# Kernel optimization log

Measured on AMD Instinct MI355X. Metric: run time of the kernel, lower is better.

Reference implementation:

```python
import jax, jax.numpy as jnp
import numpy as np

H = 1024          # hidden size
NH = 16           # num heads
HD = H // NH      # head dim = 64
I = 4096          # intermediate size
EPS = 1e-5


def _layer_norm(x, g, b):
    m = jnp.mean(x, axis=-1, keepdims=True)
    v = jnp.mean(jnp.square(x - m), axis=-1, keepdims=True)
    return (x - m) * jax.lax.rsqrt(v + EPS) * g + b


def setup_inputs() -> dict:
    key = jax.random.key(0)
    ks = jax.random.split(key, 8)
    B, S = 16, 1025
    s = 0.02
    return {
        "hidden_states": jax.random.normal(ks[0], (B, S, H), dtype=jnp.float32),
        "norm1_g": jnp.ones((H,), jnp.float32),
        "norm1_b": jnp.zeros((H,), jnp.float32),
        "qkv_w": jax.random.normal(ks[1], (3 * H, H), jnp.float32) * s,
        "qkv_b": jnp.zeros((3 * H,), jnp.float32),
        "proj_w": jax.random.normal(ks[2], (H, H), jnp.float32) * s,
        "proj_b": jnp.zeros((H,), jnp.float32),
        "ls1": jnp.full((H,), 0.1, jnp.float32),
        "norm2_g": jnp.ones((H,), jnp.float32),
        "norm2_b": jnp.zeros((H,), jnp.float32),
        "fc1_w": jax.random.normal(ks[3], (I, H), jnp.float32) * s,
        "fc1_b": jnp.zeros((I,), jnp.float32),
        "fc2_w": jax.random.normal(ks[4], (H, I), jnp.float32) * s,
        "fc2_b": jnp.zeros((H,), jnp.float32),
        "ls2": jnp.full((H,), 0.1, jnp.float32),
    }


def reference(hidden_states, norm1_g, norm1_b, qkv_w, qkv_b, proj_w, proj_b,
              ls1, norm2_g, norm2_b, fc1_w, fc1_b, fc2_w, fc2_b, ls2):
    B, S, _ = hidden_states.shape
    scale = HD ** -0.5

    # ---- attention branch ----
    x = _layer_norm(hidden_states, norm1_g, norm1_b)
    qkv = x @ qkv_w.T + qkv_b                      # [B,S,3H]
    qkv = qkv.reshape(B, S, 3, NH, HD).transpose(2, 0, 3, 1, 4)  # [3,B,NH,S,HD]
    q, k, v = qkv[0], qkv[1], qkv[2]
    attn = jnp.einsum('bhqd,bhkd->bhqk', q, k) * scale
    attn = jax.nn.softmax(attn, axis=-1)
    out = jnp.einsum('bhqk,bhkd->bhqd', attn, v)   # [B,NH,S,HD]
    out = out.transpose(0, 2, 1, 3).reshape(B, S, H)
    out = out @ proj_w.T + proj_b
    hidden_states = hidden_states + ls1 * out

    # ---- MLP branch ----
    y = _layer_norm(hidden_states, norm2_g, norm2_b)
    y = jax.nn.gelu(y @ fc1_w.T + fc1_b, approximate=False)
    y = y @ fc2_w.T + fc2_b
    return hidden_states + ls2 * y
```

## Files before the change

### kernel.cpp

```cpp
#include <hip/hip_runtime.h>

typedef __bf16 bf16_t;
typedef bf16_t bf16x8 __attribute__((ext_vector_type(8)));
typedef bf16_t bf16x4 __attribute__((ext_vector_type(4)));
typedef float f32x4 __attribute__((ext_vector_type(4)));

#define S_LEN 1025
#define B_ROWS 1032
#define M_P 16512
#define SP 1152

__global__ __launch_bounds__(256) void cvt_kernel(const float* __restrict__ qkv_w,
                                                  const float* __restrict__ proj_w,
                                                  const float* __restrict__ fc1_w,
                                                  const float* __restrict__ fc2_w,
                                                  bf16_t* __restrict__ out) {
  const int i = blockIdx.x * 256 + threadIdx.x;
  const float* src;
  int j = i;
  if (j < 786432) src = qkv_w;
  else if ((j -= 786432) < 262144) src = proj_w;
  else if ((j -= 262144) < 1048576) src = fc1_w;
  else { j -= 1048576; src = fc2_w; }
  const float4 v = ((const float4*)src)[j];
  bf16x4 o;
  o[0] = (bf16_t)v.x; o[1] = (bf16_t)v.y; o[2] = (bf16_t)v.z; o[3] = (bf16_t)v.w;
  ((bf16x4*)out)[i] = o;
}

__global__ __launch_bounds__(256) void ln_kernel(const float* __restrict__ x,
                                                 const float* __restrict__ g,
                                                 const float* __restrict__ bta,
                                                 bf16_t* __restrict__ o) {
  const int s = blockIdx.x, bb = blockIdx.y;
  const int t = threadIdx.x;
  const float4 v = ((const float4*)(x + ((long)bb * S_LEN + s) * 1024))[t];
  float sm = v.x + v.y + v.z + v.w;
  float sq = v.x * v.x + v.y * v.y + v.z * v.z + v.w * v.w;
#pragma unroll
  for (int off = 32; off > 0; off >>= 1) {
    sm += __shfl_down(sm, off);
    sq += __shfl_down(sq, off);
  }
  __shared__ float red[16];
  const int w = t >> 6, lane = t & 63;
  if (lane == 0) { red[w] = sm; red[8 + w] = sq; }
  __syncthreads();
  if (t == 0) {
    const float ts = red[0] + red[1] + red[2] + red[3];
    const float tq = red[8] + red[9] + red[10] + red[11];
    const float mean = ts * (1.0f / 1024.0f);
    const float var = tq * (1.0f / 1024.0f) - mean * mean;
    red[0] = mean;
    red[1] = rsqrtf(var + 1e-5f);
  }
  __syncthreads();
  const float mean = red[0], rstd = red[1];
  const float4 gg = ((const float4*)g)[t];
  const float4 bb2 = ((const float4*)bta)[t];
  bf16x4 ov;
  ov[0] = (bf16_t)((v.x - mean) * rstd * gg.x + bb2.x);
  ov[1] = (bf16_t)((v.y - mean) * rstd * gg.y + bb2.y);
  ov[2] = (bf16_t)((v.z - mean) * rstd * gg.z + bb2.z);
  ov[3] = (bf16_t)((v.w - mean) * rstd * gg.w + bb2.w);
  ((bf16x4*)(o + ((long)bb * B_ROWS + s) * 1024))[t] = ov;
}

enum { EPI_QKV = 0, EPI_PROJ = 1, EPI_FC2 = 3, EPI_FC1 = 2 };

template <int EPI>
__global__ __launch_bounds__(256) void gemm_bt(const bf16_t* __restrict__ A,
                                               const bf16_t* __restrict__ W,
                                               const float* __restrict__ bias,
                                               const float* __restrict__ resid,
                                               const float* __restrict__ ls,
                                               bf16_t* __restrict__ outb,
                                               float* __restrict__ outf,
                                               bf16_t* __restrict__ vt,
                                               int N, int K, int NT) {
  const int g = blockIdx.x & 7;
  const int rr = blockIdx.x >> 3;
  const int ntile = rr % NT;
  const int mloc = rr / NT;
  const int mtile = g * 17 + mloc;
  if (mtile >= 129) return;
  const int n0 = ntile * 128;
  const int m0 = mtile * 128;

  __shared__ __align__(16) char smem[34304];

  const int t = threadIdx.x;
  const int w = t >> 6;
  const int lane = t & 63;
  const int wm = (w >> 1) * 64;
  const int wn = (w & 1) * 64;
  const int ln = lane & 15;
  const int quad = lane >> 4;

  const f32x4 zero4 = {0.0f, 0.0f, 0.0f, 0.0f};
  f32x4 acc[4][4];
#pragma unroll
  for (int i = 0; i < 4; ++i)
#pragma unroll
    for (int j = 0; j < 4; ++j) acc[i][j] = zero4;

  const int r0 = t >> 2, kc0 = (t & 3) * 8;
  const int r1 = (t + 256) >> 2, kc1 = ((t + 256) & 3) * 8;
  const bf16_t* a0 = A + (long)(m0 + r0) * K + kc0;
  const bf16_t* a1 = A + (long)(m0 + r1) * K + kc1;
  const bf16_t* b0 = W + (long)(n0 + r0) * K + kc0;
  const bf16_t* b1 = W + (long)(n0 + r1) * K + kc1;

#define STAGE(KT, BUF)                                                                        \
  {                                                                                           \
    char* dA_ = smem + (BUF) * 16384;                                                         \
    char* dB_ = dA_ + 8192;                                                                   \
    __builtin_amdgcn_global_load_lds(                                                         \
        (const __attribute__((address_space(1))) void*)(a0 + (KT)),                           \
        (__attribute__((address_space(3))) void*)(dA_ + t * 16), 16, 0, 0);                   \
    __builtin_amdgcn_global_load_lds(                                                         \
        (const __attribute__((address_space(1))) void*)(a1 + (KT)),                           \
        (__attribute__((address_space(3))) void*)(dA_ + (t + 256) * 16), 16, 0, 0);           \
    __builtin_amdgcn_global_load_lds(                                                         \
        (const __attribute__((address_space(1))) void*)(b0 + (KT)),                           \
        (__attribute__((address_space(3))) void*)(dB_ + t * 16), 16, 0, 0);                   \
    __builtin_amdgcn_global_load_lds(                                                         \
        (const __attribute__((address_space(1))) void*)(b1 + (KT)),                           \
        (__attribute__((address_space(3))) void*)(dB_ + (t + 256) * 16), 16, 0, 0);           \
  }

  STAGE(0, 0)
  __syncthreads();

  int cur = 0;
  for (int kt = 32; kt <= K; kt += 32) {
    if (kt < K) STAGE(kt, cur ^ 1)
    __builtin_amdgcn_sched_barrier(0);
    const bf16_t* LA = (const bf16_t*)(smem + cur * 16384);
    const bf16_t* LB = (const bf16_t*)(smem + cur * 16384 + 8192);
    bf16x8 af[4], bfr[4];
#pragma unroll
    for (int mt = 0; mt < 4; ++mt)
      af[mt] = *(const bf16x8*)&LA[(wm + mt * 16 + ln) * 32 + quad * 8];
#pragma unroll
    for (int nt = 0; nt < 4; ++nt)
      bfr[nt] = *(const bf16x8*)&LB[(wn + nt * 16 + ln) * 32 + quad * 8];
#pragma unroll
    for (int mt = 0; mt < 4; ++mt)
#pragma unroll
      for (int nt = 0; nt < 4; ++nt)
        acc[mt][nt] = __builtin_amdgcn_mfma_f32_16x16x32_bf16(af[mt], bfr[nt], acc[mt][nt], 0, 0, 0);
    __syncthreads();
    cur ^= 1;
  }
#undef STAGE

  if (EPI == EPI_PROJ || EPI == EPI_FC2) {
    const int b0r = m0 / B_ROWS;
    const int s0 = m0 - b0r * B_ROWS;
#pragma unroll
    for (int nt = 0; nt < 4; ++nt) {
      const int n = n0 + wn + nt * 16 + ln;
      const float bn = bias[n];
      const float lsn = ls[n];
#pragma unroll
      for (int mt = 0; mt < 4; ++mt) {
#pragma unroll
        for (int r = 0; r < 4; ++r) {
          const int d = wm + mt * 16 + quad * 4 + r;
          int s = s0 + d, b = b0r;
          if (s >= B_ROWS) { s -= B_ROWS; ++b; }
          if (s < S_LEN) {
            const long idx = ((long)b * S_LEN + s) * 1024 + n;
            outf[idx] = resid[idx] + lsn * (acc[mt][nt][r] + bn);
          }
        }
      }
    }
    return;
  }

  if (EPI == EPI_QKV && n0 >= 2048) {
    bf16_t* C = (bf16_t*)smem;
#pragma unroll
    for (int nt = 0; nt < 4; ++nt) {
      const int nl = wn + nt * 16 + ln;
      const float bn = bias[n0 + nl];
#pragma unroll
      for (int mt = 0; mt < 4; ++mt)
#pragma unroll
        for (int r = 0; r < 4; ++r)
          C[nl * 134 + (wm + mt * 16 + quad * 4 + r)] = (bf16_t)(acc[mt][nt][r] + bn);
    }
    __syncthreads();
    const int b0r = m0 / B_ROWS;
    const int s0 = m0 - b0r * B_ROWS;
#pragma unroll
    for (int p = 0; p < 8; ++p) {
      const int nl = p * 16 + (t >> 4);
      const int sc = (t & 15) * 8;
      const int n = n0 + nl;
      const int h = (n >> 6) - 32, d = n & 63;
      int s = s0 + sc, b = b0r;
      if (s >= B_ROWS) { s -= B_ROWS; ++b; }
      *(bf16x8*)&vt[(((long)b * 16 + h) * 64 + d) * (long)SP + s] =
          *(const bf16x8*)&C[nl * 134 + sc];
    }
    return;
  }

  {
    bf16_t* C = (bf16_t*)smem;
#pragma unroll
    for (int nt = 0; nt < 4; ++nt) {
      const int nl = wn + nt * 16 + ln;
      const float bn = bias[n0 + nl];
#pragma unroll
      for (int mt = 0; mt < 4; ++mt)
#pragma unroll
        for (int r = 0; r < 4; ++r) {
          float c = acc[mt][nt][r] + bn;
          if (EPI == EPI_FC1) c = c / (1.0f + __expf(-1.702f * c));
          C[(wm + mt * 16 + quad * 4 + r) * 132 + nl] = (bf16_t)c;
        }
    }
    __syncthreads();
    const long stride = (EPI == EPI_QKV) ? 2048 : N;
#pragma unroll
    for (int p = 0; p < 8; ++p) {
      const int row = p * 16 + (t >> 4);
      const int sc = (t & 15) * 8;
      *(bf16x8*)&outb[(long)(m0 + row) * stride + n0 + sc] = *(const bf16x8*)&C[row * 132 + sc];
    }
  }
}

#define SCL 0.18033688f

__global__ __launch_bounds__(256) void attn_kernel(const bf16_t* __restrict__ qk,
                                                   const bf16_t* __restrict__ vt,
                                                   bf16_t* __restrict__ out) {
  const int g = blockIdx.x & 7;
  const int idx = blockIdx.x >> 3;
  const int bh = g * 32 + idx / 17;
  const int q0 = (idx % 17) * 64;
  const int b = bh >> 4, h = bh & 15;
  const int t = threadIdx.x;
  const int wv = t >> 6, lane = t & 63;
  const int ln = lane & 15, quad = lane >> 4;

  __shared__ __align__(16) char smem[35840];
  bf16_t* ldsK = (bf16_t*)smem;
  bf16_t* ldsP = (bf16_t*)smem;
  bf16_t* ldsV = (bf16_t*)(smem + 18432);

  const long rowbase = (long)b * B_ROWS;

  int qrow = q0 + wv * 16 + ln;
  if (qrow > S_LEN - 1) qrow = S_LEN - 1;
  const bf16_t* qp = qk + (rowbase + qrow) * 2048 + h * 64;
  const bf16x8 qf0 = *(const bf16x8*)(qp + quad * 8);
  const bf16x8 qf1 = *(const bf16x8*)(qp + 32 + quad * 8);

  const bf16_t* vbase = vt + (long)bh * 64 * SP;

  const f32x4 zero4 = {0.0f, 0.0f, 0.0f, 0.0f};
  f32x4 oacc[4];
  float l_part[4] = {0.0f, 0.0f, 0.0f, 0.0f};
#pragma unroll
  for (int i = 0; i < 4; ++i) oacc[i] = zero4;

  for (int k0 = 0; k0 < 1152; k0 += 128) {
    __syncthreads();
#pragma unroll
    for (int i = 0; i < 4; ++i) {
      const int slot = t + i * 256;
      const int key = slot >> 3, ch = (slot & 7) * 8;
      int krow = k0 + key;
      if (krow > S_LEN - 1) krow = S_LEN - 1;
      *(bf16x8*)&ldsK[key * 72 + ch] =
          *(const bf16x8*)(qk + (rowbase + krow) * 2048 + 1024 + h * 64 + ch);
    }
#pragma unroll
    for (int i = 0; i < 4; ++i) {
      const int slot = t + i * 256;
      const int dim = slot >> 4, kc = (slot & 15) * 8;
      *(bf16x8*)&ldsV[dim * 136 + kc] = *(const bf16x8*)(vbase + (long)dim * SP + k0 + kc);
    }
    __syncthreads();

    f32x4 s[8];
#pragma unroll
    for (int nt = 0; nt < 8; ++nt) {
      const bf16x8 kf0 = *(const bf16x8*)&ldsK[(nt * 16 + ln) * 72 + quad * 8];
      const bf16x8 kf1 = *(const bf16x8*)&ldsK[(nt * 16 + ln) * 72 + 32 + quad * 8];
      f32x4 a = zero4;
      a = __builtin_amdgcn_mfma_f32_16x16x32_bf16(qf0, kf0, a, 0, 0, 0);
      a = __builtin_amdgcn_mfma_f32_16x16x32_bf16(qf1, kf1, a, 0, 0, 0);
#pragma unroll
      for (int r = 0; r < 4; ++r) s[nt][r] = a[r] * SCL;
    }
    if (k0 + 128 > S_LEN) {
#pragma unroll
      for (int nt = 0; nt < 8; ++nt) {
        const bool valid = (k0 + nt * 16 + ln) < S_LEN;
#pragma unroll
        for (int r = 0; r < 4; ++r) s[nt][r] = valid ? s[nt][r] : -1e30f;
      }
    }
    __syncthreads();

    bf16_t* P = ldsP + wv * 2176;
#pragma unroll
    for (int nt = 0; nt < 8; ++nt)
#pragma unroll
      for (int r = 0; r < 4; ++r) {
        const float p = exp2f(s[nt][r]);
        l_part[r] += p;
        P[(quad * 4 + r) * 136 + nt * 16 + ln] = (bf16_t)p;
      }

#pragma unroll
    for (int ko = 0; ko < 4; ++ko) {
      const bf16x8 pf = *(const bf16x8*)&P[ln * 136 + ko * 32 + quad * 8];
#pragma unroll
      for (int dt = 0; dt < 4; ++dt) {
        const bf16x8 vf = *(const bf16x8*)&ldsV[(dt * 16 + ln) * 136 + ko * 32 + quad * 8];
        oacc[dt] = __builtin_amdgcn_mfma_f32_16x16x32_bf16(pf, vf, oacc[dt], 0, 0, 0);
      }
    }
  }

#pragma unroll
  for (int off = 1; off < 16; off <<= 1)
#pragma unroll
    for (int r = 0; r < 4; ++r) l_part[r] += __shfl_xor(l_part[r], off);

#pragma unroll
  for (int r = 0; r < 4; ++r) {
    const int q = q0 + wv * 16 + quad * 4 + r;
    if (q < S_LEN) {
      const float inv = 1.0f / l_part[r];
#pragma unroll
      for (int dt = 0; dt < 4; ++dt)
        out[(rowbase + q) * 1024 + h * 64 + dt * 16 + ln] = (bf16_t)(oacc[dt][r] * inv);
    }
  }
}

extern "C" void kernel_launch(void* const* d_in, const int* in_sizes, int n_in,
                              void* d_out, int out_size, void* d_ws, size_t ws_size,
                              hipStream_t stream) {
  (void)in_sizes; (void)n_in; (void)out_size; (void)ws_size;
  const float* hidden = (const float*)d_in[0];
  const float* n1g = (const float*)d_in[1];
  const float* n1b = (const float*)d_in[2];
  const float* qkv_w = (const float*)d_in[3];
  const float* qkv_b = (const float*)d_in[4];
  const float* proj_w = (const float*)d_in[5];
  const float* proj_b = (const float*)d_in[6];
  const float* ls1 = (const float*)d_in[7];
  const float* n2g = (const float*)d_in[8];
  const float* n2b = (const float*)d_in[9];
  const float* fc1_w = (const float*)d_in[10];
  const float* fc1_b = (const float*)d_in[11];
  const float* fc2_w = (const float*)d_in[12];
  const float* fc2_b = (const float*)d_in[13];
  const float* ls2 = (const float*)d_in[14];
  float* out = (float*)d_out;

  char* ws = (char*)d_ws;
  bf16_t* R1 = (bf16_t*)ws;
  char* shared = ws + 33816576L;
  bf16_t* qkbuf = (bf16_t*)shared;
  bf16_t* vtbuf = (bf16_t*)(shared + 67633152L);
  bf16_t* gelu = (bf16_t*)shared;
  bf16_t* wqkv = (bf16_t*)(ws + 33816576L + 135266304L);
  bf16_t* wproj = wqkv + 3145728;
  bf16_t* wfc1 = wproj + 1048576;
  bf16_t* wfc2 = wfc1 + 4194304;

  cvt_kernel<<<12288, 256, 0, stream>>>(qkv_w, proj_w, fc1_w, fc2_w, wqkv);

  ln_kernel<<<dim3(S_LEN, 16), 256, 0, stream>>>(hidden, n1g, n1b, R1);

  gemm_bt<EPI_QKV><<<136 * 24, 256, 0, stream>>>(R1, wqkv, qkv_b, nullptr, nullptr,
                                                 qkbuf, nullptr, vtbuf, 3072, 1024, 24);

  attn_kernel<<<4352, 256, 0, stream>>>(qkbuf, vtbuf, R1);

  gemm_bt<EPI_PROJ><<<136 * 8, 256, 0, stream>>>(R1, wproj, proj_b, hidden, ls1,
                                                 nullptr, out, nullptr, 1024, 1024, 8);

  ln_kernel<<<dim3(S_LEN, 16), 256, 0, stream>>>(out, n2g, n2b, R1);

  gemm_bt<EPI_FC1><<<136 * 32, 256, 0, stream>>>(R1, wfc1, fc1_b, nullptr, nullptr,
                                                 gelu, nullptr, nullptr, 4096, 1024, 32);

  gemm_bt<EPI_FC2><<<136 * 8, 256, 0, stream>>>(gelu, wfc2, fc2_b, out, ls2,
                                                nullptr, out, nullptr, 1024, 4096, 8);
}
```

Measured before the change: 1.113 ms.

## Use four-slot LDS ring with prefetch depth two and XOR-swizzled layout in GEMM

Replaces the double-buffered K loop in the bf16 GEMM with a four-slot shared-memory ring that prefetches two tiles ahead, waiting on vmcnt instead of a full sync every iteration. The global-to-LDS destination columns are XOR-swizzled by row so fragment reads avoid bank conflicts. MFMA issue gets raised wave priority. This costs 64KB of LDS per block, which may lower occupancy, and the trailing dummy loads at offset 0 add some extra traffic.

New measurement: 1.074 ms. 1.04x faster.

```diff
diff --git a/kernel.cpp b/kernel.cpp
--- a/kernel.cpp
+++ b/kernel.cpp
@@ -87,7 +87,7 @@
   const int n0 = ntile * 128;
   const int m0 = mtile * 128;
 
-  __shared__ __align__(16) char smem[34304];
+  __shared__ __align__(16) char smem[65536];
 
   const int t = threadIdx.x;
   const int w = t >> 6;
@@ -104,16 +104,19 @@
 #pragma unroll
     for (int j = 0; j < 4; ++j) acc[i][j] = zero4;
 
-  const int r0 = t >> 2, kc0 = (t & 3) * 8;
-  const int r1 = (t + 256) >> 2, kc1 = ((t + 256) & 3) * 8;
-  const bf16_t* a0 = A + (long)(m0 + r0) * K + kc0;
-  const bf16_t* a1 = A + (long)(m0 + r1) * K + kc1;
-  const bf16_t* b0 = W + (long)(n0 + r0) * K + kc0;
-  const bf16_t* b1 = W + (long)(n0 + r1) * K + kc1;
-
-#define STAGE(KT, BUF)                                                                        \
+  const int sr0 = t >> 2, sr1 = (t + 256) >> 2;
+  const int sc0 = (t & 3) ^ ((sr0 >> 1) & 3);
+  const int sc1 = (t & 3) ^ ((sr1 >> 1) & 3);
+  const bf16_t* a0 = A + (long)(m0 + sr0) * K + sc0 * 8;
+  const bf16_t* a1 = A + (long)(m0 + sr1) * K + sc1 * 8;
+  const bf16_t* b0 = W + (long)(n0 + sr0) * K + sc0 * 8;
+  const bf16_t* b1 = W + (long)(n0 + sr1) * K + sc1 * 8;
+
+  const int laneOff = ln * 64 + ((quad ^ ((ln >> 1) & 3)) << 4);
+
+#define STAGE(KT, RING)                                                                       \
   {                                                                                           \
-    char* dA_ = smem + (BUF) * 16384;                                                         \
+    char* dA_ = smem + (RING) * 16384;                                                        \
     char* dB_ = dA_ + 8192;                                                                   \
     __builtin_amdgcn_global_load_lds(                                                         \
         (const __attribute__((address_space(1))) void*)(a0 + (KT)),                           \
@@ -130,30 +133,38 @@
   }
 
   STAGE(0, 0)
-  __syncthreads();
-
-  int cur = 0;
-  for (int kt = 32; kt <= K; kt += 32) {
-    if (kt < K) STAGE(kt, cur ^ 1)
+  STAGE(32, 1)
+
+  const int NTILES = K >> 5;
+  for (int T = 0; T < NTILES; ++T) {
+    asm volatile("s_waitcnt vmcnt(4)" ::: "memory");
+    __builtin_amdgcn_s_barrier();
     __builtin_amdgcn_sched_barrier(0);
-    const bf16_t* LA = (const bf16_t*)(smem + cur * 16384);
-    const bf16_t* LB = (const bf16_t*)(smem + cur * 16384 + 8192);
+
+    const char* ringA = smem + (T & 3) * 16384;
+    const char* ringB = ringA + 8192;
     bf16x8 af[4], bfr[4];
 #pragma unroll
     for (int mt = 0; mt < 4; ++mt)
-      af[mt] = *(const bf16x8*)&LA[(wm + mt * 16 + ln) * 32 + quad * 8];
+      af[mt] = *(const bf16x8*)(ringA + (wm + mt * 16) * 64 + laneOff);
 #pragma unroll
     for (int nt = 0; nt < 4; ++nt)
-      bfr[nt] = *(const bf16x8*)&LB[(wn + nt * 16 + ln) * 32 + quad * 8];
+      bfr[nt] = *(const bf16x8*)(ringB + (wn + nt * 16) * 64 + laneOff);
+
+    const int kt2 = (T + 2 < NTILES) ? (T + 2) * 32 : 0;
+    STAGE(kt2, (T + 2) & 3)
+    __builtin_amdgcn_sched_barrier(0);
+
+    __builtin_amdgcn_s_setprio(1);
 #pragma unroll
     for (int mt = 0; mt < 4; ++mt)
 #pragma unroll
       for (int nt = 0; nt < 4; ++nt)
         acc[mt][nt] = __builtin_amdgcn_mfma_f32_16x16x32_bf16(af[mt], bfr[nt], acc[mt][nt], 0, 0, 0);
-    __syncthreads();
-    cur ^= 1;
+    __builtin_amdgcn_s_setprio(0);
   }
 #undef STAGE
+  __syncthreads();
 
   if (EPI == EPI_PROJ || EPI == EPI_FC2) {
     const int b0r = m0 / B_ROWS;
```
